# Performance work log

Measured on AMD Instinct MI355X. Metric: run time of the kernel, lower is better.

## Reference

```python
import jax, jax.numpy as jnp
import numpy as np

WIDTH_POW = 10
WIDTH = 2 ** WIDTH_POW          # 1024
HALF = WIDTH // 2               # 512
DEPTH = 32
BATCH = 32768


def setup_inputs() -> dict:
    key = jax.random.key(0)
    kx, ks, kr = jax.random.split(key, 3)
    X = jax.random.normal(kx, (BATCH, WIDTH), dtype=jnp.float32)
    # Replicate the torch init: rand_sgn * (1 - rand/depth) / 2 + 0.5
    rand_sgn = (jax.random.randint(ks, (HALF, DEPTH), 0, 2) * 2 - 1).astype(jnp.float32)
    u = jax.random.uniform(kr, (HALF, DEPTH), dtype=jnp.float32)
    params = rand_sgn * (1.0 - u / DEPTH) / 2.0 + 0.5
    return {"X": X, "params": params}


def reference(X, params):
    """Doubly stochastic butterfly: at each depth step, each feature pair
    (j, j+half) is mixed by the 2x2 doubly stochastic block [[1-w, w], [w, 1-w]]
    with w = params[j, i]. Vectorized over batch; depth handled by lax.scan."""
    half = params.shape[0]

    def step(x, w):
        # x: [B, 2*half], w: [half]
        x0 = x[:, :half]
        x1 = x[:, half:]
        new_x0 = x0 * (1.0 - w) + x1 * w
        new_x1 = x1 * (1.0 - w) + x0 * w
        return jnp.concatenate([new_x0, new_x1], axis=1), None

    out, _ = jax.lax.scan(step, X, params.T)  # scan over depth axis
    return out
```

## Files before the change

kernel.cpp:

```cpp
#include <hip/hip_runtime.h>

#define WIDTH 1024
#define HALF  512
#define DEPTH 32
#define BATCH 32768

__global__ void butterfly_gains(const float* __restrict__ params,
                                float* __restrict__ g) {
    int j = blockIdx.x * blockDim.x + threadIdx.x;
    if (j < HALF) {
        const float* p = params + (long long)j * DEPTH;
        float prod = 1.0f;
#pragma unroll
        for (int i = 0; i < DEPTH; ++i) {
            prod *= (1.0f - 2.0f * p[i]);
        }
        g[j] = prod;
    }
}

__global__ void __launch_bounds__(256)
butterfly_apply(const float* __restrict__ X,
                const float* __restrict__ g,
                float* __restrict__ out) {
    const int PAIRS4 = HALF / 4;
    long long idx = (long long)blockIdx.x * blockDim.x + threadIdx.x;
    int b  = (int)(idx >> 7);
    int jv = (int)(idx & 127);

    const float4* x0p = (const float4*)(X + (long long)b * WIDTH);
    const float4* x1p = (const float4*)(X + (long long)b * WIDTH + HALF);
    float4 x0 = x0p[jv];
    float4 x1 = x1p[jv];
    float4 gv = ((const float4*)g)[jv];

    float4 o0, o1;
    {
        float h = 0.5f * (x0.x + x1.x);
        float e = 0.5f * (x0.x - x1.x) * gv.x;
        o0.x = h + e; o1.x = h - e;
    }
    {
        float h = 0.5f * (x0.y + x1.y);
        float e = 0.5f * (x0.y - x1.y) * gv.y;
        o0.y = h + e; o1.y = h - e;
    }
    {
        float h = 0.5f * (x0.z + x1.z);
        float e = 0.5f * (x0.z - x1.z) * gv.z;
        o0.z = h + e; o1.z = h - e;
    }
    {
        float h = 0.5f * (x0.w + x1.w);
        float e = 0.5f * (x0.w - x1.w) * gv.w;
        o0.w = h + e; o1.w = h - e;
    }

    float4* o0p = (float4*)(out + (long long)b * WIDTH);
    float4* o1p = (float4*)(out + (long long)b * WIDTH + HALF);
    o0p[jv] = o0;
    o1p[jv] = o1;
}

extern "C" void kernel_launch(void* const* d_in, const int* in_sizes, int n_in,
                              void* d_out, int out_size, void* d_ws, size_t ws_size,
                              hipStream_t stream) {
    const float* X      = (const float*)d_in[0];
    const float* params = (const float*)d_in[1];
    float* out = (float*)d_out;
    float* g   = (float*)d_ws;

    hipLaunchKernelGGL(butterfly_gains, dim3(2), dim3(256), 0, stream, params, g);

    const long long total = (long long)BATCH * (HALF / 4);
    const int threads = 256;
    const int blocks = (int)((total + threads - 1) / threads);
    hipLaunchKernelGGL(butterfly_apply, dim3(blocks), dim3(threads), 0, stream,
                       X, g, out);
}
```

Measured before the change: 231.2 us.

## Fuse gain computation into a grid-stride apply kernel with nontemporal I/O

Merges the two launches into one kernel. Each block recomputes the 512 per-pair gains into shared memory, then grid-strides over the batch with a fixed 2048-block grid. Input loads and output stores use nontemporal builtins to avoid polluting cache on this streaming workload. Each block now redoes the gain products (64 KB of params reads per block), and the shared-memory barrier delays the start of streaming.

```diff
diff --git a/kernel.cpp b/kernel.cpp
--- a/kernel.cpp
+++ b/kernel.cpp
@@ -1,65 +1,59 @@
 #include <hip/hip_runtime.h>
 
-#define WIDTH 1024
-#define HALF  512
-#define DEPTH 32
-#define BATCH 32768
+#define WIDTH  1024
+#define HALF   512
+#define DEPTH  32
+#define BATCH  32768
+#define PAIRS4 (HALF / 4)
+#define NTHREADS 256
+#define NBLOCKS  2048
 
-__global__ void butterfly_gains(const float* __restrict__ params,
-                                float* __restrict__ g) {
-    int j = blockIdx.x * blockDim.x + threadIdx.x;
-    if (j < HALF) {
-        const float* p = params + (long long)j * DEPTH;
+typedef float f4 __attribute__((ext_vector_type(4)));
+
+__global__ void __launch_bounds__(NTHREADS)
+butterfly_fused(const float* __restrict__ X,
+                const float* __restrict__ params,
+                float* __restrict__ out) {
+    __shared__ float gs[HALF];
+
+    const int tid = threadIdx.x;
+
+    for (int j = tid; j < HALF; j += NTHREADS) {
+        const float* p = params + j * DEPTH;
         float prod = 1.0f;
 #pragma unroll
         for (int i = 0; i < DEPTH; ++i) {
             prod *= (1.0f - 2.0f * p[i]);
         }
-        g[j] = prod;
+        gs[j] = prod;
     }
-}
+    __syncthreads();
 
-__global__ void __launch_bounds__(256)
-butterfly_apply(const float* __restrict__ X,
-                const float* __restrict__ g,
-                float* __restrict__ out) {
-    const int PAIRS4 = HALF / 4;
-    long long idx = (long long)blockIdx.x * blockDim.x + threadIdx.x;
-    int b  = (int)(idx >> 7);
-    int jv = (int)(idx & 127);
+    const long long total = (long long)BATCH * PAIRS4;
+    const long long stride = (long long)NBLOCKS * NTHREADS;
 
-    const float4* x0p = (const float4*)(X + (long long)b * WIDTH);
-    const float4* x1p = (const float4*)(X + (long long)b * WIDTH + HALF);
-    float4 x0 = x0p[jv];
-    float4 x1 = x1p[jv];
-    float4 gv = ((const float4*)g)[jv];
+    for (long long idx = (long long)blockIdx.x * NTHREADS + tid;
+         idx < total; idx += stride) {
+        const int b  = (int)(idx >> 7);
+        const int jv = (int)(idx & 127);
 
-    float4 o0, o1;
-    {
-        float h = 0.5f * (x0.x + x1.x);
-        float e = 0.5f * (x0.x - x1.x) * gv.x;
-        o0.x = h + e; o1.x = h - e;
+        const f4* x0p = (const f4*)(X + (long long)b * WIDTH);
+        const f4* x1p = x0p + PAIRS4;
+
+        f4 x0 = __builtin_nontemporal_load(x0p + jv);
+        f4 x1 = __builtin_nontemporal_load(x1p + jv);
+        f4 gv = ((const f4*)gs)[jv];
+
+        f4 h = 0.5f * (x0 + x1);
+        f4 e = 0.5f * (x0 - x1) * gv;
+        f4 o0 = h + e;
+        f4 o1 = h - e;
+
+        f4* o0p = (f4*)(out + (long long)b * WIDTH);
+        f4* o1p = o0p + PAIRS4;
+        __builtin_nontemporal_store(o0, o0p + jv);
+        __builtin_nontemporal_store(o1, o1p + jv);
     }
-    {
-        float h = 0.5f * (x0.y + x1.y);
-        float e = 0.5f * (x0.y - x1.y) * gv.y;
-        o0.y = h + e; o1.y = h - e;
-    }
-    {
-        float h = 0.5f * (x0.z + x1.z);
-        float e = 0.5f * (x0.z - x1.z) * gv.z;
-        o0.z = h + e; o1.z = h - e;
-    }
-    {
-        float h = 0.5f * (x0.w + x1.w);
-        float e = 0.5f * (x0.w - x1.w) * gv.w;
-        o0.w = h + e; o1.w = h - e;
-    }
-
-    float4* o0p = (float4*)(out + (long long)b * WIDTH);
-    float4* o1p = (float4*)(out + (long long)b * WIDTH + HALF);
-    o0p[jv] = o0;
-    o1p[jv] = o1;
 }
 
 extern "C" void kernel_launch(void* const* d_in, const int* in_sizes, int n_in,
@@ -68,13 +62,7 @@
     const float* X      = (const float*)d_in[0];
     const float* params = (const float*)d_in[1];
     float* out = (float*)d_out;
-    float* g   = (float*)d_ws;
 
-    hipLaunchKernelGGL(butterfly_gains, dim3(2), dim3(256), 0, stream, params, g);
-
-    const long long total = (long long)BATCH * (HALF / 4);
-    const int threads = 256;
-    const int blocks = (int)((total + threads - 1) / threads);
-    hipLaunchKernelGGL(butterfly_apply, dim3(blocks), dim3(threads), 0, stream,
-                       X, g, out);
+    hipLaunchKernelGGL(butterfly_fused, dim3(NBLOCKS), dim3(NTHREADS), 0, stream,
+                       X, params, out);
 }
```

After: 230.6 us. Within noise of the previous version (-0.3%).
